# Kernel optimization log

Hardware: AMD Instinct MI355X
Metric: run time of the kernel (lower is better)

## Reference

```python
import jax, jax.numpy as jnp
import numpy as np

N_HEAD = 16
D_MODEL = 1024


def setup_inputs() -> dict:
    key = jax.random.key(0)
    k1, k2, k3, k4, k5, k6 = jax.random.split(key, 6)
    B, S, D = 2, 2048, D_MODEL
    src = jax.random.normal(k1, (B, S, D), dtype=jnp.float32)
    attn_mask = jax.random.uniform(k2, (B, S, S), dtype=jnp.float32)
    # torch nn.Linear(d, 3d) / nn.Linear(d, d) params; stored as (in, out) for x @ W
    scale = 1.0 / np.sqrt(D)
    W_qkv = jax.random.uniform(k3, (D, 3 * D), dtype=jnp.float32, minval=-scale, maxval=scale)
    b_qkv = jax.random.uniform(k4, (3 * D,), dtype=jnp.float32, minval=-scale, maxval=scale)
    W_out = jax.random.uniform(k5, (D, D), dtype=jnp.float32, minval=-scale, maxval=scale)
    b_out = jax.random.uniform(k6, (D,), dtype=jnp.float32, minval=-scale, maxval=scale)
    return {"src": src, "attn_mask": attn_mask, "W_qkv": W_qkv, "b_qkv": b_qkv,
            "W_out": W_out, "b_out": b_out}


def reference(src, attn_mask, W_qkv, b_qkv, W_out, b_out):
    B, S, D = src.shape
    H = N_HEAD
    dh = D // H
    # broadcast mask [B,S,S] -> [B,1,S,S] (matches torch unsqueeze(1))
    mask = attn_mask[:, None, :, :]
    qkv = src @ W_qkv + b_qkv                      # [B,S,3D]
    q, k, v = jnp.split(qkv, 3, axis=-1)
    q = q.reshape(B, S, H, dh).transpose(0, 2, 1, 3)   # [B,H,S,dh]
    k = k.reshape(B, S, H, dh).transpose(0, 2, 1, 3)
    v = v.reshape(B, S, H, dh).transpose(0, 2, 1, 3)
    scores = jnp.einsum('bhqd,bhkd->bhqk', q, k) * (float(dh) ** -0.5)
    scores = scores * mask + (mask - 1.0) * 10000.0
    weights = jax.nn.softmax(scores, axis=-1)      # dropout_p=0 -> identity in eval/train
    out = jnp.einsum('bhqk,bhkd->bhqd', weights, v)
    out = out.transpose(0, 2, 1, 3).reshape(B, S, D)
    return out @ W_out + b_out
```

## Files before the change

kernel.cpp:

```cpp
#include <hip/hip_runtime.h>
#include <stdint.h>

#define SEQ    2048
#define DMODEL 1024

typedef __bf16 bf16x8 __attribute__((ext_vector_type(8)));
typedef float  f32x4  __attribute__((ext_vector_type(4)));

typedef __attribute__((address_space(1))) const void CGV;
typedef __attribute__((address_space(3))) void LDSV;

__device__ __forceinline__ void load_lds16(const void* g, void* l) {
    __builtin_amdgcn_global_load_lds((CGV*)g, (LDSV*)l, 16, 0, 0);
}

__device__ __forceinline__ float fast_exp2(float x) { return __builtin_exp2f(x); }

__global__ __launch_bounds__(256)
void transpose_f32_to_bf16(const float* __restrict__ in, __bf16* __restrict__ out,
                           int R, int C)
{
    __shared__ float tile[32][33];
    const int t  = threadIdx.x;
    const int tx = t & 31, ty = t >> 5;
    const int c0 = blockIdx.x * 32;
    const int r0 = blockIdx.y * 32;
#pragma unroll
    for (int i = 0; i < 4; ++i)
        tile[ty + i * 8][tx] = in[(size_t)(r0 + ty + i * 8) * C + c0 + tx];
    __syncthreads();
#pragma unroll
    for (int i = 0; i < 4; ++i)
        out[(size_t)(c0 + ty + i * 8) * R + r0 + tx] = (__bf16)tile[tx][ty + i * 8];
}

__global__ __launch_bounds__(256)
void convert_f32_to_bf16(const float* __restrict__ in, __bf16* __restrict__ out)
{
    const int i = (blockIdx.x * 256 + threadIdx.x) * 8;
    float4 a = *(const float4*)(in + i);
    float4 b = *(const float4*)(in + i + 4);
    __bf16 tmp[8] = { (__bf16)a.x, (__bf16)a.y, (__bf16)a.z, (__bf16)a.w,
                      (__bf16)b.x, (__bf16)b.y, (__bf16)b.z, (__bf16)b.w };
    *(uint4*)(out + i) = *(uint4*)tmp;
}

__global__ __launch_bounds__(256)
void transpose_v(const __bf16* __restrict__ in, __bf16* __restrict__ out)
{
    __shared__ __bf16 tile[32][34];
    const int t  = threadIdx.x;
    const int tx = t & 31, ty = t >> 5;
    const int s0 = blockIdx.x * 32;
    const int d0 = blockIdx.y * 32;
    const int bh = blockIdx.z;
    const __bf16* ip = in  + (size_t)bh * SEQ * 64;
    __bf16*       op = out + (size_t)bh * 64 * SEQ;
#pragma unroll
    for (int i = 0; i < 4; ++i)
        tile[ty + i * 8][tx] = ip[(size_t)(s0 + ty + i * 8) * 64 + d0 + tx];
    __syncthreads();
#pragma unroll
    for (int i = 0; i < 4; ++i)
        op[(size_t)(d0 + ty + i * 8) * SEQ + s0 + tx] = tile[tx][ty + i * 8];
}

__global__ __launch_bounds__(256)
void gemm_kernel(const __bf16* __restrict__ A, const __bf16* __restrict__ Bt,
                 const float* __restrict__ bias,
                 __bf16* __restrict__ Cq, __bf16* __restrict__ Ck,
                 __bf16* __restrict__ Cv, float* __restrict__ Cplain,
                 int K, int N, int mode)
{
    __shared__ __attribute__((aligned(16))) __bf16 As[2][128][32];
    __shared__ __attribute__((aligned(16))) __bf16 Bs[2][128][32];

    const int t    = threadIdx.x;
    const int wave = __builtin_amdgcn_readfirstlane(t >> 6);
    const int lane = t & 63;
    const int l15  = lane & 15;
    const int quad = lane >> 4;
    const int wm   = (wave >> 1) * 64;
    const int wn   = (wave & 1) * 64;
    const int m0   = blockIdx.y * 128;
    const int n0   = blockIdx.x * 128;

    const int arow  = lane >> 2;
    const int akoff = (lane & 3) * 8;

    f32x4 acc[4][4] = {};

#define GSTAGE(buf, kk)                                                        \
    {                                                                          \
        _Pragma("unroll")                                                      \
        for (int p = 0; p < 2; ++p) {                                          \
            int slab = (wave * 2 + p) * 16;                                    \
            load_lds16(A  + (size_t)(m0 + slab + arow) * K + (kk) + akoff,     \
                       &As[buf][slab][0]);                                     \
            load_lds16(Bt + (size_t)(n0 + slab + arow) * K + (kk) + akoff,     \
                       &Bs[buf][slab][0]);                                     \
        }                                                                      \
    }

    GSTAGE(0, 0);
    int cur = 0;
#pragma unroll 2
    for (int k0 = 0; k0 < K; k0 += 32) {
        asm volatile("s_waitcnt vmcnt(0)" ::: "memory");
        __builtin_amdgcn_s_barrier();
        __builtin_amdgcn_sched_barrier(0);
        if (k0 + 32 < K) GSTAGE(cur ^ 1, k0 + 32);
        __builtin_amdgcn_sched_barrier(0);

        bf16x8 af[4], bfr[4];
#pragma unroll
        for (int mi = 0; mi < 4; ++mi)
            af[mi] = *(const bf16x8*)(&As[cur][wm + mi * 16 + l15][quad * 8]);
#pragma unroll
        for (int ni = 0; ni < 4; ++ni)
            bfr[ni] = *(const bf16x8*)(&Bs[cur][wn + ni * 16 + l15][quad * 8]);
#pragma unroll
        for (int mi = 0; mi < 4; ++mi)
#pragma unroll
            for (int ni = 0; ni < 4; ++ni)
                acc[mi][ni] = __builtin_amdgcn_mfma_f32_16x16x32_bf16(
                    af[mi], bfr[ni], acc[mi][ni], 0, 0, 0);
        cur ^= 1;
    }
#undef GSTAGE

#pragma unroll
    for (int mi = 0; mi < 4; ++mi) {
        int rowb = m0 + wm + mi * 16 + quad * 4;
#pragma unroll
        for (int ni = 0; ni < 4; ++ni) {
            int col = n0 + wn + ni * 16 + l15;
            float bia = bias[col];
#pragma unroll
            for (int r = 0; r < 4; ++r) {
                float v = acc[mi][ni][r] + bia;
                int rr = rowb + r;
                if (mode == 0) {
                    int b = rr >> 11;
                    int s = rr & 2047;
                    int part = col >> 10;
                    int rem  = col & 1023;
                    int h = rem >> 6;
                    int d = rem & 63;
                    __bf16* dst = (part == 0) ? Cq : (part == 1) ? Ck : Cv;
                    dst[(((size_t)(b * 16 + h)) * SEQ + s) * 64 + d] = (__bf16)v;
                } else {
                    Cplain[(size_t)rr * N + col] = v;
                }
            }
        }
    }
}

__global__ __launch_bounds__(128, 2)
void attn_kernel(const __bf16* __restrict__ Q, const __bf16* __restrict__ Kb,
                 const __bf16* __restrict__ Vtg, const float* __restrict__ mask,
                 __bf16* __restrict__ Out)
{
    __shared__ __attribute__((aligned(16))) __bf16 Kt[2][64 * 64];
    __shared__ __attribute__((aligned(16))) __bf16 Vt[2][64 * 64];
    __shared__ __attribute__((aligned(16))) __bf16 Ps[2][32 * 64];

    const int t    = threadIdx.x;
    const int wave = __builtin_amdgcn_readfirstlane(t >> 6);
    const int lane = t & 63;
    const int l15  = lane & 15;
    const int quad = lane >> 4;
    const int swq  = lane & 7;
    const int bh   = blockIdx.x;
    const int b    = bh >> 4;
    const int h    = bh & 15;
    const int q0   = blockIdx.y * 64 + wave * 32;

    const float C1 = 0.180336880f;
    const float C2 = 14426.9502f;

    const __bf16* Qp  = Q   + (size_t)bh * SEQ * 64;
    const __bf16* Kp  = Kb  + (size_t)bh * SEQ * 64;
    const __bf16* Vtp = Vtg + (size_t)bh * 64 * SEQ;
    const float*  Mrow0 = mask + (size_t)b * SEQ * SEQ + (size_t)(q0 + l15) * SEQ + quad * 4;
    const float*  Mrow1 = Mrow0 + (size_t)16 * SEQ;

    const int swz = ((lane & 7) ^ (lane >> 3)) * 8;
    const __bf16* kS[4];
    const __bf16* vS[4];
#pragma unroll
    for (int p = 0; p < 4; ++p) {
        int rw = wave * 32 + p * 8 + (lane >> 3);
        kS[p] = Kp  + (size_t)rw * 64 + swz;
        vS[p] = Vtp + (size_t)rw * SEQ + swz;
    }

    bf16x8 qf00, qf01, qf10, qf11;
    qf00 = *(const bf16x8*)(Qp + (size_t)(q0 + l15) * 64 + quad * 8);
    qf01 = *(const bf16x8*)(Qp + (size_t)(q0 + l15) * 64 + 32 + quad * 8);
    qf10 = *(const bf16x8*)(Qp + (size_t)(q0 + 16 + l15) * 64 + quad * 8);
    qf11 = *(const bf16x8*)(Qp + (size_t)(q0 + 16 + l15) * 64 + 32 + quad * 8);

    f32x4 oacc0[4] = {}, oacc1[4] = {};
    float mrun0 = -1e30f, lrun0 = 0.f;
    float mrun1 = -1e30f, lrun1 = 0.f;

#define STAGE_KV(bufidx, key)                                                 \
    {                                                                         \
        _Pragma("unroll")                                                     \
        for (int p = 0; p < 4; ++p) {                                         \
            load_lds16(kS[p] + (size_t)(key) * 64,                            \
                       &Kt[bufidx][(wave * 4 + p) * 512]);                    \
            load_lds16(vS[p] + (key), &Vt[bufidx][(wave * 4 + p) * 512]);     \
        }                                                                     \
    }

    STAGE_KV(0, 0);
    f32x4 mk0[4], mk1[4];
#pragma unroll
    for (int nb = 0; nb < 4; ++nb) {
        mk0[nb] = *(const f32x4*)(Mrow0 + nb * 16);
        mk1[nb] = *(const f32x4*)(Mrow1 + nb * 16);
    }

    const char* PsW0 = (const char*)&Ps[wave][0] + l15 * 128;
    const char* PsW1 = PsW0 + 16 * 128;

#pragma unroll 2
    for (int tt = 0; tt < SEQ / 64; ++tt) {
        const int key0 = tt * 64;
        const int keyn = (key0 + 64 <= SEQ - 64) ? key0 + 64 : SEQ - 64;
        const int cur  = tt & 1;
        const char* kcur = (const char*)&Kt[cur][0];
        const char* vcur = (const char*)&Vt[cur][0];

        asm volatile("s_waitcnt vmcnt(8)" ::: "memory");
        __builtin_amdgcn_s_barrier();
        __builtin_amdgcn_sched_barrier(0);

        if (tt < SEQ / 64 - 1) STAGE_KV(cur ^ 1, key0 + 64);
        __builtin_amdgcn_sched_barrier(0);

        f32x4 sa0[4], sa1[4];
#pragma unroll
        for (int nb = 0; nb < 4; ++nb) {
            const char* kb = kcur + (nb * 16 + l15) * 128;
            bf16x8 kf0 = *(const bf16x8*)(kb + (((quad) ^ swq) << 4));
            bf16x8 kf1 = *(const bf16x8*)(kb + (((4 + quad) ^ swq) << 4));
            f32x4 z0 = {}, z1 = {};
            z0 = __builtin_amdgcn_mfma_f32_16x16x32_bf16(kf0, qf00, z0, 0, 0, 0);
            z1 = __builtin_amdgcn_mfma_f32_16x16x32_bf16(kf0, qf10, z1, 0, 0, 0);
            z0 = __builtin_amdgcn_mfma_f32_16x16x32_bf16(kf1, qf01, z0, 0, 0, 0);
            z1 = __builtin_amdgcn_mfma_f32_16x16x32_bf16(kf1, qf11, z1, 0, 0, 0);
            sa0[nb] = z0;
            sa1[nb] = z1;
        }

#pragma unroll
        for (int nb = 0; nb < 4; ++nb)
#pragma unroll
            for (int r = 0; r < 4; ++r) {
                float t0 = __fmaf_rn(C1, sa0[nb][r], C2);
                float t1 = __fmaf_rn(C1, sa1[nb][r], C2);
                sa0[nb][r] = __fmaf_rn(mk0[nb][r], t0, -C2);
                sa1[nb][r] = __fmaf_rn(mk1[nb][r], t1, -C2);
            }
#pragma unroll
        for (int nb = 0; nb < 4; ++nb) {
            mk0[nb] = *(const f32x4*)(Mrow0 + keyn + nb * 16);
            mk1[nb] = *(const f32x4*)(Mrow1 + keyn + nb * 16);
        }

        float v0 = fmaxf(fmaxf(sa0[0][0], sa0[0][1]), fmaxf(sa0[0][2], sa0[0][3]));
        float v1 = fmaxf(fmaxf(sa1[0][0], sa1[0][1]), fmaxf(sa1[0][2], sa1[0][3]));
#pragma unroll
        for (int nb = 1; nb < 4; ++nb) {
            v0 = fmaxf(v0, fmaxf(fmaxf(sa0[nb][0], sa0[nb][1]), fmaxf(sa0[nb][2], sa0[nb][3])));
            v1 = fmaxf(v1, fmaxf(fmaxf(sa1[nb][0], sa1[nb][1]), fmaxf(sa1[nb][2], sa1[nb][3])));
        }
        v0 = fmaxf(v0, __shfl_xor(v0, 16));
        v1 = fmaxf(v1, __shfl_xor(v1, 16));
        v0 = fmaxf(v0, __shfl_xor(v0, 32));
        v1 = fmaxf(v1, __shfl_xor(v1, 32));

        float al0 = 1.f, al1 = 1.f;
        bool need = (v0 > mrun0 + 8.f) || (v1 > mrun1 + 8.f);
        if (__any(need)) {
            float nm0 = fmaxf(mrun0, v0);
            float nm1 = fmaxf(mrun1, v1);
            al0 = fast_exp2(mrun0 - nm0);
            al1 = fast_exp2(mrun1 - nm1);
            mrun0 = nm0;
            mrun1 = nm1;
            float a0[4], a1[4];
#pragma unroll
            for (int r = 0; r < 4; ++r) {
                a0[r] = __shfl(al0, quad * 4 + r);
                a1[r] = __shfl(al1, quad * 4 + r);
            }
#pragma unroll
            for (int cb = 0; cb < 4; ++cb)
#pragma unroll
                for (int r = 0; r < 4; ++r) {
                    oacc0[cb][r] *= a0[r];
                    oacc1[cb][r] *= a1[r];
                }
        }

        float ac0 = 0.f, ac1 = 0.f;
#pragma unroll
        for (int nb = 0; nb < 4; ++nb)
#pragma unroll
            for (int r = 0; r < 4; ++r) {
                float p0 = fast_exp2(sa0[nb][r] - mrun0);
                float p1 = fast_exp2(sa1[nb][r] - mrun1);
                sa0[nb][r] = p0;
                sa1[nb][r] = p1;
                ac0 += p0;
                ac1 += p1;
            }
        ac0 += __shfl_xor(ac0, 16);
        ac1 += __shfl_xor(ac1, 16);
        ac0 += __shfl_xor(ac0, 32);
        ac1 += __shfl_xor(ac1, 32);
        lrun0 = lrun0 * al0 + ac0;
        lrun1 = lrun1 * al1 + ac1;

#pragma unroll
        for (int nb = 0; nb < 4; ++nb) {
            union { __bf16 hh[4]; uint2 u; } p0, p1;
            p0.hh[0] = (__bf16)sa0[nb][0];
            p0.hh[1] = (__bf16)sa0[nb][1];
            p0.hh[2] = (__bf16)sa0[nb][2];
            p0.hh[3] = (__bf16)sa0[nb][3];
            p1.hh[0] = (__bf16)sa1[nb][0];
            p1.hh[1] = (__bf16)sa1[nb][1];
            p1.hh[2] = (__bf16)sa1[nb][2];
            p1.hh[3] = (__bf16)sa1[nb][3];
            const int so = (((nb * 2 + (quad >> 1)) ^ swq) << 4) + (quad & 1) * 8;
            *(uint2*)(PsW0 + so) = p0.u;
            *(uint2*)(PsW1 + so) = p1.u;
        }
        asm volatile("s_waitcnt lgkmcnt(0)" ::: "memory");
        __builtin_amdgcn_sched_barrier(0);

        bf16x8 pf00 = *(const bf16x8*)(PsW0 + (((quad) ^ swq) << 4));
        bf16x8 pf01 = *(const bf16x8*)(PsW0 + (((4 + quad) ^ swq) << 4));
        bf16x8 pf10 = *(const bf16x8*)(PsW1 + (((quad) ^ swq) << 4));
        bf16x8 pf11 = *(const bf16x8*)(PsW1 + (((4 + quad) ^ swq) << 4));

        __builtin_amdgcn_s_setprio(1);
#pragma unroll
        for (int cb = 0; cb < 4; ++cb) {
            const char* vb = vcur + (cb * 16 + l15) * 128;
            bf16x8 vf0 = *(const bf16x8*)(vb + (((quad) ^ swq) << 4));
            bf16x8 vf1 = *(const bf16x8*)(vb + (((4 + quad) ^ swq) << 4));
            oacc0[cb] = __builtin_amdgcn_mfma_f32_16x16x32_bf16(pf00, vf0, oacc0[cb], 0, 0, 0);
            oacc1[cb] = __builtin_amdgcn_mfma_f32_16x16x32_bf16(pf10, vf0, oacc1[cb], 0, 0, 0);
            oacc0[cb] = __builtin_amdgcn_mfma_f32_16x16x32_bf16(pf01, vf1, oacc0[cb], 0, 0, 0);
            oacc1[cb] = __builtin_amdgcn_mfma_f32_16x16x32_bf16(pf11, vf1, oacc1[cb], 0, 0, 0);
        }
        __builtin_amdgcn_s_setprio(0);
    }
#undef STAGE_KV

    float l40[4], l41[4];
#pragma unroll
    for (int r = 0; r < 4; ++r) {
        l40[r] = __shfl(lrun0, quad * 4 + r);
        l41[r] = __shfl(lrun1, quad * 4 + r);
    }
#pragma unroll
    for (int cb = 0; cb < 4; ++cb) {
#pragma unroll
        for (int r = 0; r < 4; ++r) {
            int qq0 = q0 + quad * 4 + r;
            Out[((size_t)(b * SEQ + qq0)) * DMODEL + h * 64 + cb * 16 + l15] =
                (__bf16)(oacc0[cb][r] / l40[r]);
            Out[((size_t)(b * SEQ + qq0 + 16)) * DMODEL + h * 64 + cb * 16 + l15] =
                (__bf16)(oacc1[cb][r] / l41[r]);
        }
    }
}

extern "C" void kernel_launch(void* const* d_in, const int* in_sizes, int n_in,
                              void* d_out, int out_size, void* d_ws, size_t ws_size,
                              hipStream_t stream)
{
    const float* src  = nullptr;
    const float* mask = nullptr;
    const float* Wqkv = nullptr;
    const float* bqkv = nullptr;
    const float* Wout = nullptr;
    const float* bout = nullptr;
    for (int i = 0; i < n_in; ++i) {
        switch (in_sizes[i]) {
            case 4194304: src  = (const float*)d_in[i]; break;
            case 8388608: mask = (const float*)d_in[i]; break;
            case 3145728: Wqkv = (const float*)d_in[i]; break;
            case 3072:    bqkv = (const float*)d_in[i]; break;
            case 1048576: Wout = (const float*)d_in[i]; break;
            case 1024:    bout = (const float*)d_in[i]; break;
        }
    }
    float* out = (float*)d_out;

    const size_t NE = (size_t)2 * 16 * SEQ * 64;
    __bf16* Qb     = (__bf16*)d_ws;
    __bf16* Kb     = Qb + NE;
    __bf16* Vb     = Kb + NE;
    __bf16* Vtg    = Vb + NE;
    __bf16* Wqkv_t = Vtg + NE;
    __bf16* Wout_t = Wqkv_t + (size_t)3072 * 1024;
    __bf16* Ao     = Vb;
    __bf16* SrcBf  = Vtg;

    transpose_f32_to_bf16<<<dim3(3072 / 32, 1024 / 32), 256, 0, stream>>>(
        Wqkv, Wqkv_t, 1024, 3072);
    transpose_f32_to_bf16<<<dim3(1024 / 32, 1024 / 32), 256, 0, stream>>>(
        Wout, Wout_t, 1024, 1024);

    convert_f32_to_bf16<<<dim3(4194304 / (256 * 8)), 256, 0, stream>>>(src, SrcBf);

    gemm_kernel<<<dim3(3072 / 128, 4096 / 128), 256, 0, stream>>>(
        SrcBf, Wqkv_t, bqkv, Qb, Kb, Vb, nullptr, 1024, 3072, 0);

    transpose_v<<<dim3(SEQ / 32, 2, 32), 256, 0, stream>>>(Vb, Vtg);

    attn_kernel<<<dim3(32, SEQ / 64), 128, 0, stream>>>(Qb, Kb, Vtg, mask, Ao);

    gemm_kernel<<<dim3(1024 / 128, 4096 / 128), 256, 0, stream>>>(
        Ao, Wout_t, bout, nullptr, nullptr, nullptr, out, 1024, 1024, 1);
}
```

Baseline: 265.1 us.

## Load K/V fragments directly from global into registers, drop LDS staging

Removes the LDS double-buffered K/V staging with async global-to-LDS loads and barriers. Each wave instead loads its MFMA K and V fragments straight from global memory into registers, prefetching the next tile while computing the current one. Blocks grow to 4 waves covering 128 queries. This drops barrier and LDS traffic, but every wave now fetches K/V independently, which multiplies global/L2 reads and raises register pressure.

```diff
diff --git a/kernel.cpp b/kernel.cpp
--- a/kernel.cpp
+++ b/kernel.cpp
@@ -157,14 +157,12 @@
     }
 }
 
-__global__ __launch_bounds__(128, 2)
+__global__ __launch_bounds__(256, 2)
 void attn_kernel(const __bf16* __restrict__ Q, const __bf16* __restrict__ Kb,
                  const __bf16* __restrict__ Vtg, const float* __restrict__ mask,
                  __bf16* __restrict__ Out)
 {
-    __shared__ __attribute__((aligned(16))) __bf16 Kt[2][64 * 64];
-    __shared__ __attribute__((aligned(16))) __bf16 Vt[2][64 * 64];
-    __shared__ __attribute__((aligned(16))) __bf16 Ps[2][32 * 64];
+    __shared__ __attribute__((aligned(16))) __bf16 Ps[4][32 * 64];
 
     const int t    = threadIdx.x;
     const int wave = __builtin_amdgcn_readfirstlane(t >> 6);
@@ -175,7 +173,7 @@
     const int bh   = blockIdx.x;
     const int b    = bh >> 4;
     const int h    = bh & 15;
-    const int q0   = blockIdx.y * 64 + wave * 32;
+    const int q0   = blockIdx.y * 128 + wave * 32;
 
     const float C1 = 0.180336880f;
     const float C2 = 14426.9502f;
@@ -186,75 +184,57 @@
     const float*  Mrow0 = mask + (size_t)b * SEQ * SEQ + (size_t)(q0 + l15) * SEQ + quad * 4;
     const float*  Mrow1 = Mrow0 + (size_t)16 * SEQ;
 
-    const int swz = ((lane & 7) ^ (lane >> 3)) * 8;
-    const __bf16* kS[4];
-    const __bf16* vS[4];
-#pragma unroll
-    for (int p = 0; p < 4; ++p) {
-        int rw = wave * 32 + p * 8 + (lane >> 3);
-        kS[p] = Kp  + (size_t)rw * 64 + swz;
-        vS[p] = Vtp + (size_t)rw * SEQ + swz;
-    }
-
-    bf16x8 qf00, qf01, qf10, qf11;
-    qf00 = *(const bf16x8*)(Qp + (size_t)(q0 + l15) * 64 + quad * 8);
-    qf01 = *(const bf16x8*)(Qp + (size_t)(q0 + l15) * 64 + 32 + quad * 8);
-    qf10 = *(const bf16x8*)(Qp + (size_t)(q0 + 16 + l15) * 64 + quad * 8);
-    qf11 = *(const bf16x8*)(Qp + (size_t)(q0 + 16 + l15) * 64 + 32 + quad * 8);
+    const __bf16* Kfb = Kp  + (size_t)l15 * 64 + quad * 8;
+    const __bf16* Vfb = Vtp + (size_t)l15 * SEQ + quad * 8;
+
+    bf16x8 qf00 = *(const bf16x8*)(Qp + (size_t)(q0 + l15) * 64 + quad * 8);
+    bf16x8 qf01 = *(const bf16x8*)(Qp + (size_t)(q0 + l15) * 64 + 32 + quad * 8);
+    bf16x8 qf10 = *(const bf16x8*)(Qp + (size_t)(q0 + 16 + l15) * 64 + quad * 8);
+    bf16x8 qf11 = *(const bf16x8*)(Qp + (size_t)(q0 + 16 + l15) * 64 + 32 + quad * 8);
 
     f32x4 oacc0[4] = {}, oacc1[4] = {};
     float mrun0 = -1e30f, lrun0 = 0.f;
     float mrun1 = -1e30f, lrun1 = 0.f;
 
-#define STAGE_KV(bufidx, key)                                                 \
-    {                                                                         \
-        _Pragma("unroll")                                                     \
-        for (int p = 0; p < 4; ++p) {                                         \
-            load_lds16(kS[p] + (size_t)(key) * 64,                            \
-                       &Kt[bufidx][(wave * 4 + p) * 512]);                    \
-            load_lds16(vS[p] + (key), &Vt[bufidx][(wave * 4 + p) * 512]);     \
-        }                                                                     \
-    }
-
-    STAGE_KV(0, 0);
-    f32x4 mk0[4], mk1[4];
+    bf16x8 kf[4][2], vf[4][2];
+    f32x4  mk0[4], mk1[4];
+#pragma unroll
+    for (int nb = 0; nb < 4; ++nb) {
+        kf[nb][0] = *(const bf16x8*)(Kfb + (size_t)(nb * 16) * 64);
+        kf[nb][1] = *(const bf16x8*)(Kfb + (size_t)(nb * 16) * 64 + 32);
+    }
 #pragma unroll
     for (int nb = 0; nb < 4; ++nb) {
         mk0[nb] = *(const f32x4*)(Mrow0 + nb * 16);
         mk1[nb] = *(const f32x4*)(Mrow1 + nb * 16);
     }
+#pragma unroll
+    for (int cb = 0; cb < 4; ++cb) {
+        vf[cb][0] = *(const bf16x8*)(Vfb + (size_t)(cb * 16) * SEQ);
+        vf[cb][1] = *(const bf16x8*)(Vfb + (size_t)(cb * 16) * SEQ + 32);
+    }
 
     const char* PsW0 = (const char*)&Ps[wave][0] + l15 * 128;
     const char* PsW1 = PsW0 + 16 * 128;
 
-#pragma unroll 2
     for (int tt = 0; tt < SEQ / 64; ++tt) {
-        const int key0 = tt * 64;
-        const int keyn = (key0 + 64 <= SEQ - 64) ? key0 + 64 : SEQ - 64;
-        const int cur  = tt & 1;
-        const char* kcur = (const char*)&Kt[cur][0];
-        const char* vcur = (const char*)&Vt[cur][0];
-
-        asm volatile("s_waitcnt vmcnt(8)" ::: "memory");
-        __builtin_amdgcn_s_barrier();
-        __builtin_amdgcn_sched_barrier(0);
-
-        if (tt < SEQ / 64 - 1) STAGE_KV(cur ^ 1, key0 + 64);
-        __builtin_amdgcn_sched_barrier(0);
+        const int keyn = (tt + 1 < SEQ / 64) ? (tt + 1) * 64 : tt * 64;
 
         f32x4 sa0[4], sa1[4];
 #pragma unroll
         for (int nb = 0; nb < 4; ++nb) {
-            const char* kb = kcur + (nb * 16 + l15) * 128;
-            bf16x8 kf0 = *(const bf16x8*)(kb + (((quad) ^ swq) << 4));
-            bf16x8 kf1 = *(const bf16x8*)(kb + (((4 + quad) ^ swq) << 4));
             f32x4 z0 = {}, z1 = {};
-            z0 = __builtin_amdgcn_mfma_f32_16x16x32_bf16(kf0, qf00, z0, 0, 0, 0);
-            z1 = __builtin_amdgcn_mfma_f32_16x16x32_bf16(kf0, qf10, z1, 0, 0, 0);
-            z0 = __builtin_amdgcn_mfma_f32_16x16x32_bf16(kf1, qf01, z0, 0, 0, 0);
-            z1 = __builtin_amdgcn_mfma_f32_16x16x32_bf16(kf1, qf11, z1, 0, 0, 0);
+            z0 = __builtin_amdgcn_mfma_f32_16x16x32_bf16(kf[nb][0], qf00, z0, 0, 0, 0);
+            z1 = __builtin_amdgcn_mfma_f32_16x16x32_bf16(kf[nb][0], qf10, z1, 0, 0, 0);
+            z0 = __builtin_amdgcn_mfma_f32_16x16x32_bf16(kf[nb][1], qf01, z0, 0, 0, 0);
+            z1 = __builtin_amdgcn_mfma_f32_16x16x32_bf16(kf[nb][1], qf11, z1, 0, 0, 0);
             sa0[nb] = z0;
             sa1[nb] = z1;
+        }
+#pragma unroll
+        for (int nb = 0; nb < 4; ++nb) {
+            kf[nb][0] = *(const bf16x8*)(Kfb + (size_t)(keyn + nb * 16) * 64);
+            kf[nb][1] = *(const bf16x8*)(Kfb + (size_t)(keyn + nb * 16) * 64 + 32);
         }
 
 #pragma unroll
@@ -353,17 +333,19 @@
         __builtin_amdgcn_s_setprio(1);
 #pragma unroll
         for (int cb = 0; cb < 4; ++cb) {
-            const char* vb = vcur + (cb * 16 + l15) * 128;
-            bf16x8 vf0 = *(const bf16x8*)(vb + (((quad) ^ swq) << 4));
-            bf16x8 vf1 = *(const bf16x8*)(vb + (((4 + quad) ^ swq) << 4));
-            oacc0[cb] = __builtin_amdgcn_mfma_f32_16x16x32_bf16(pf00, vf0, oacc0[cb], 0, 0, 0);
-            oacc1[cb] = __builtin_amdgcn_mfma_f32_16x16x32_bf16(pf10, vf0, oacc1[cb], 0, 0, 0);
-            oacc0[cb] = __builtin_amdgcn_mfma_f32_16x16x32_bf16(pf01, vf1, oacc0[cb], 0, 0, 0);
-            oacc1[cb] = __builtin_amdgcn_mfma_f32_16x16x32_bf16(pf11, vf1, oacc1[cb], 0, 0, 0);
+            oacc0[cb] = __builtin_amdgcn_mfma_f32_16x16x32_bf16(pf00, vf[cb][0], oacc0[cb], 0, 0, 0);
+            oacc1[cb] = __builtin_amdgcn_mfma_f32_16x16x32_bf16(pf10, vf[cb][0], oacc1[cb], 0, 0, 0);
+            oacc0[cb] = __builtin_amdgcn_mfma_f32_16x16x32_bf16(pf01, vf[cb][1], oacc0[cb], 0, 0, 0);
+            oacc1[cb] = __builtin_amdgcn_mfma_f32_16x16x32_bf16(pf11, vf[cb][1], oacc1[cb], 0, 0, 0);
         }
         __builtin_amdgcn_s_setprio(0);
-    }
-#undef STAGE_KV
+
+#pragma unroll
+        for (int cb = 0; cb < 4; ++cb) {
+            vf[cb][0] = *(const bf16x8*)(Vfb + (size_t)(cb * 16) * SEQ + keyn);
+            vf[cb][1] = *(const bf16x8*)(Vfb + (size_t)(cb * 16) * SEQ + keyn + 32);
+        }
+    }
 
     float l40[4], l41[4];
 #pragma unroll
@@ -428,7 +410,7 @@
 
     transpose_v<<<dim3(SEQ / 32, 2, 32), 256, 0, stream>>>(Vb, Vtg);
 
-    attn_kernel<<<dim3(32, SEQ / 64), 128, 0, stream>>>(Qb, Kb, Vtg, mask, Ao);
+    attn_kernel<<<dim3(32, SEQ / 128), 256, 0, stream>>>(Qb, Kb, Vtg, mask, Ao);
 
     gemm_kernel<<<dim3(1024 / 128, 4096 / 128), 256, 0, stream>>>(
         Ao, Wout_t, bout, nullptr, nullptr, nullptr, out, 1024, 1024, 1);
```

Result: slower. 342.0 us (+29.0%).
